# Performance work log

Hardware: AMD Instinct MI355X
Metric: run time of the kernel (lower is better)

## Reference

```python
import jax, jax.numpy as jnp
import numpy as np

FACTOR = 1.0

def _dct_matrix():
    n = 8
    D = np.zeros((n * n, n * n), dtype=np.float32)
    for u in range(n):
        for v in range(n):
            au = 1.0 / np.sqrt(2.0) if u == 0 else 1.0
            av = 1.0 / np.sqrt(2.0) if v == 0 else 1.0
            alpha = au * av * 0.25
            for x in range(n):
                for y in range(n):
                    D[u * n + v, x * n + y] = alpha * np.cos((2 * x + 1) * u * np.pi / 16) * np.cos((2 * y + 1) * v * np.pi / 16)
    return D

def _y_quant_table():
    t = np.array([[16, 11, 10, 16, 24, 40, 51, 61], [12, 12, 14, 19, 26, 58, 60, 55],
                  [14, 13, 16, 24, 40, 57, 69, 56], [14, 17, 22, 29, 51, 87, 80, 62],
                  [18, 22, 37, 56, 68, 109, 103, 77], [24, 35, 55, 64, 81, 104, 113, 92],
                  [49, 64, 78, 87, 103, 121, 120, 101], [72, 92, 95, 98, 112, 100, 103, 99]],
                 dtype=np.float32).T
    return t

def _c_quant_table():
    t = np.full((8, 8), 99, dtype=np.float32)
    t[:4, :4] = np.array([[17, 18, 24, 47], [18, 21, 26, 66], [24, 26, 56, 99], [47, 66, 99, 99]],
                          dtype=np.float32).T
    return t

_D = jnp.asarray(_dct_matrix())          # [64,64]
_QT = jnp.stack([jnp.asarray(_y_quant_table()),
                 jnp.asarray(_c_quant_table()),
                 jnp.asarray(_c_quant_table())], axis=0) * FACTOR  # [3,8,8]

def setup_inputs() -> dict:
    key = jax.random.key(0)
    image = jax.random.uniform(key, (32, 3, 512, 512), dtype=jnp.float32)
    return {"image": image}

def _diffjpeg(image):
    x = jnp.clip(image, 0.0, 1.0)
    B, C, H, W = x.shape  # H, W multiples of 8 -> no padding branch
    r, g, b = x[:, 0], x[:, 1], x[:, 2]
    y = 0.299 * r + 0.587 * g + 0.114 * b
    cb = (b - y) * 0.564 + 0.5
    cr = (r - y) * 0.713 + 0.5
    ycbcr = jnp.stack([y, cb, cr], axis=1)  # [B,3,H,W]
    # blockify into 8x8 tiles
    nh, nw = H // 8, W // 8
    blocks = ycbcr.reshape(B, C, nh, 8, nw, 8).transpose(0, 1, 2, 4, 3, 5)  # [B,C,nh,nw,8,8]
    flat = blocks.reshape(-1, 64) * 255.0 - 128.0
    dct = flat @ _D.T                      # matmul(D, flat.T).T
    dctb = dct.reshape(B, C, nh, nw, 8, 8)
    qte = _QT[None, :, None, None, :, :]   # [1,3,1,1,8,8]
    q = dctb / qte
    q = q + jax.lax.stop_gradient(jnp.round(q) - q)  # STE rounding
    deq = q * qte
    idct = deq.reshape(-1, 64) @ _D        # matmul(D.T, x.T).T
    idct = (idct + 128.0) / 255.0
    img = idct.reshape(B, C, nh, nw, 8, 8).transpose(0, 1, 2, 4, 3, 5).reshape(B, C, H, W)
    yy, ycb, ycr = img[:, 0], img[:, 1] - 0.5, img[:, 2] - 0.5
    rr = yy + 1.403 * ycr
    gg = yy - 0.714 * ycr - 0.344 * ycb
    bb = yy + 1.773 * ycb
    rgb = jnp.clip(jnp.stack([rr, gg, bb], axis=1), 0.0, 1.0)
    return jnp.clip(rgb, 0.0, 1.0)

def reference(image):
    return _diffjpeg(image)
```

## Files before the change

### kernel.cpp

```cpp
#include <hip/hip_runtime.h>

typedef float f32x2 __attribute__((ext_vector_type(2)));

#define K4 0.353553391f
#define K1 0.490392640f
#define K3 0.415734806f
#define K5 0.277785117f
#define K7 0.097545161f
#define K2 0.461939766f
#define K6 0.191341716f

__device__ __align__(16) const float YQT[64] = {
    16.f, 12.f, 14.f, 14.f,  18.f,  24.f,  49.f,  72.f,
    11.f, 12.f, 13.f, 17.f,  22.f,  35.f,  64.f,  92.f,
    10.f, 14.f, 16.f, 22.f,  37.f,  55.f,  78.f,  95.f,
    16.f, 19.f, 24.f, 29.f,  56.f,  64.f,  87.f,  98.f,
    24.f, 26.f, 40.f, 51.f,  68.f,  81.f, 103.f, 112.f,
    40.f, 58.f, 57.f, 87.f, 109.f, 104.f, 121.f, 100.f,
    51.f, 60.f, 69.f, 80.f, 103.f, 113.f, 120.f, 103.f,
    61.f, 55.f, 56.f, 62.f,  77.f,  92.f, 101.f,  99.f
};
__device__ __align__(16) const float RYQT[64] = {
    1.f/16.f, 1.f/12.f, 1.f/14.f, 1.f/14.f, 1.f/18.f,  1.f/24.f,  1.f/49.f,  1.f/72.f,
    1.f/11.f, 1.f/12.f, 1.f/13.f, 1.f/17.f, 1.f/22.f,  1.f/35.f,  1.f/64.f,  1.f/92.f,
    1.f/10.f, 1.f/14.f, 1.f/16.f, 1.f/22.f, 1.f/37.f,  1.f/55.f,  1.f/78.f,  1.f/95.f,
    1.f/16.f, 1.f/19.f, 1.f/24.f, 1.f/29.f, 1.f/56.f,  1.f/64.f,  1.f/87.f,  1.f/98.f,
    1.f/24.f, 1.f/26.f, 1.f/40.f, 1.f/51.f, 1.f/68.f,  1.f/81.f,  1.f/103.f, 1.f/112.f,
    1.f/40.f, 1.f/58.f, 1.f/57.f, 1.f/87.f, 1.f/109.f, 1.f/104.f, 1.f/121.f, 1.f/100.f,
    1.f/51.f, 1.f/60.f, 1.f/69.f, 1.f/80.f, 1.f/103.f, 1.f/113.f, 1.f/120.f, 1.f/103.f,
    1.f/61.f, 1.f/55.f, 1.f/56.f, 1.f/62.f, 1.f/77.f,  1.f/92.f,  1.f/101.f, 1.f/99.f
};
__device__ __align__(16) const float CQ[64] = {
    17.f, 18.f, 24.f, 47.f, 99.f, 99.f, 99.f, 99.f,
    18.f, 21.f, 26.f, 66.f, 99.f, 99.f, 99.f, 99.f,
    24.f, 26.f, 56.f, 99.f, 99.f, 99.f, 99.f, 99.f,
    47.f, 66.f, 99.f, 99.f, 99.f, 99.f, 99.f, 99.f,
    99.f, 99.f, 99.f, 99.f, 99.f, 99.f, 99.f, 99.f,
    99.f, 99.f, 99.f, 99.f, 99.f, 99.f, 99.f, 99.f,
    99.f, 99.f, 99.f, 99.f, 99.f, 99.f, 99.f, 99.f,
    99.f, 99.f, 99.f, 99.f, 99.f, 99.f, 99.f, 99.f
};
__device__ __align__(16) const float RCQ[64] = {
    1.f/17.f, 1.f/18.f, 1.f/24.f, 1.f/47.f, 1.f/99.f, 1.f/99.f, 1.f/99.f, 1.f/99.f,
    1.f/18.f, 1.f/21.f, 1.f/26.f, 1.f/66.f, 1.f/99.f, 1.f/99.f, 1.f/99.f, 1.f/99.f,
    1.f/24.f, 1.f/26.f, 1.f/56.f, 1.f/99.f, 1.f/99.f, 1.f/99.f, 1.f/99.f, 1.f/99.f,
    1.f/47.f, 1.f/66.f, 1.f/99.f, 1.f/99.f, 1.f/99.f, 1.f/99.f, 1.f/99.f, 1.f/99.f,
    1.f/99.f, 1.f/99.f, 1.f/99.f, 1.f/99.f, 1.f/99.f, 1.f/99.f, 1.f/99.f, 1.f/99.f,
    1.f/99.f, 1.f/99.f, 1.f/99.f, 1.f/99.f, 1.f/99.f, 1.f/99.f, 1.f/99.f, 1.f/99.f,
    1.f/99.f, 1.f/99.f, 1.f/99.f, 1.f/99.f, 1.f/99.f, 1.f/99.f, 1.f/99.f, 1.f/99.f,
    1.f/99.f, 1.f/99.f, 1.f/99.f, 1.f/99.f, 1.f/99.f, 1.f/99.f, 1.f/99.f, 1.f/99.f
};

__device__ __forceinline__ float gfma(float a, float b, float c) { return fmaf(a, b, c); }
__device__ __forceinline__ f32x2 gfma(f32x2 a, f32x2 b, f32x2 c) { return __builtin_elementwise_fma(a, b, c); }
__device__ __forceinline__ f32x2 gfma(float a, f32x2 b, f32x2 c) { return __builtin_elementwise_fma((f32x2){a, a}, b, c); }

__device__ __forceinline__ float clamp01(float x) { return __builtin_amdgcn_fmed3f(x, 0.f, 1.f); }

template <typename T>
__device__ __forceinline__ void dct8(const T x[8], T X[8]) {
    const T a0 = x[0] + x[7], a1 = x[1] + x[6], a2 = x[2] + x[5], a3 = x[3] + x[4];
    const T d0 = x[0] - x[7], d1 = x[1] - x[6], d2 = x[2] - x[5], d3 = x[3] - x[4];
    const T e0 = a0 + a3, e1 = a1 + a2, f0 = a0 - a3, f1 = a1 - a2;
    X[0] = K4 * (e0 + e1);
    X[4] = K4 * (e0 - e1);
    X[2] = gfma(K6, f1, K2 * f0);
    X[6] = gfma(-K2, f1, K6 * f0);
    X[1] = gfma(K7, d3, gfma(K5, d2, gfma(K3, d1, K1 * d0)));
    X[3] = gfma(-K5, d3, gfma(-K1, d2, gfma(-K7, d1, K3 * d0)));
    X[5] = gfma(K3, d3, gfma(K7, d2, gfma(-K1, d1, K5 * d0)));
    X[7] = gfma(-K1, d3, gfma(K3, d2, gfma(-K5, d1, K7 * d0)));
}

template <typename T>
__device__ __forceinline__ void idct8(const T X[8], T x[8]) {
    const T g0 = K4 * (X[0] + X[4]);
    const T g1 = K4 * (X[0] - X[4]);
    const T E0 = gfma(K6, X[6], gfma(K2, X[2], g0));
    const T E1 = gfma(-K2, X[6], gfma(K6, X[2], g1));
    const T E2 = gfma(K2, X[6], gfma(-K6, X[2], g1));
    const T E3 = gfma(-K6, X[6], gfma(-K2, X[2], g0));
    const T O0 = gfma(K7, X[7], gfma(K5, X[5], gfma(K3, X[3], K1 * X[1])));
    const T O1 = gfma(-K5, X[7], gfma(-K1, X[5], gfma(-K7, X[3], K3 * X[1])));
    const T O2 = gfma(K3, X[7], gfma(K7, X[5], gfma(-K1, X[3], K5 * X[1])));
    const T O3 = gfma(-K1, X[7], gfma(K3, X[5], gfma(-K5, X[3], K7 * X[1])));
    x[0] = E0 + O0;  x[7] = E0 - O0;
    x[1] = E1 + O1;  x[6] = E1 - O1;
    x[2] = E2 + O2;  x[5] = E2 - O2;
    x[3] = E3 + O3;  x[4] = E3 - O3;
}

__device__ __forceinline__ f32x2 quant2(f32x2 sv, f32x2 qt, f32x2 rq) {
    const f32x2 q0 = sv * rq;
    const f32x2 e  = gfma(-qt, q0, sv);
    const f32x2 q  = gfma(rq, e, q0);
    const f32x2 n  = {rintf(q.x), rintf(q.y)};
    return n * qt;
}

#define SB() __builtin_amdgcn_sched_barrier(0)

#define YW 68
#define CW 70

__global__ __launch_bounds__(128, 8) void diffjpeg_kernel(const float* __restrict__ in,
                                                          float* __restrict__ out)
{
    __shared__ __align__(16) f32x2 lds[2][8][CW];

    const int t  = threadIdx.x;
    const int l  = t & 63;
    const int wv = t >> 6;
    const int b8 = (l >> 3) * 8;
    const int rr = l & 7;

    f32x2 (*plc)[CW] = lds[wv];
    float* ply = (float*)&lds[wv][0][0];

    const int bid  = blockIdx.x;
    const int img  = bid >> 8;
    const int rem  = bid & 255;
    const int trow = rem >> 3;
    const int tcol = rem & 7;
    const size_t HW = (size_t)512 * 512;
    const size_t sbase = (size_t)img * 3 * HW + (size_t)(trow * 16 + wv * 8) * 512 + (size_t)(tcol * 64);
    const float* __restrict__ pin  = in  + sbase + l;
    float* __restrict__       pout = out + sbase + l;

    float rv[8], gv[8], bv[8];
    #pragma unroll
    for (int x = 0; x < 8; ++x) rv[x] = pin[(size_t)x * 512];
    #pragma unroll
    for (int x = 0; x < 8; ++x) gv[x] = pin[HW + (size_t)x * 512];
    #pragma unroll
    for (int x = 0; x < 8; ++x) bv[x] = pin[2 * HW + (size_t)x * 512];

    float yv[8];
    f32x2 cc[8];
    #pragma unroll
    for (int x = 0; x < 8; ++x) {
        const float r = clamp01(rv[x]);
        const float g = clamp01(gv[x]);
        const float b = clamp01(bv[x]);
        const float Y = fmaf(76.245f, r, fmaf(149.685f, g, 29.07f * b));
        yv[x] = Y - 128.f;
        const f32x2 tbr = gfma(255.f, (f32x2){b, r}, (f32x2){-Y, -Y});
        cc[x] = gfma((f32x2){0.564f, 0.713f}, tbr, (f32x2){-0.5f, -0.5f});
    }

    float sy[8];
    {
        float X0[8];
        dct8(yv, X0);
        #pragma unroll
        for (int u = 0; u < 8; ++u) ply[u * YW + l] = X0[u];
        SB();

        {
            const float4* yq4  = (const float4*)&YQT[rr * 8];
            const float4* ryq4 = (const float4*)&RYQT[rr * 8];
            const float4 yqa = yq4[0],  yqb = yq4[1];
            const float4 rya = ryq4[0], ryb = ryq4[1];
            const float yq[8]  = {yqa.x, yqa.y, yqa.z, yqa.w, yqb.x, yqb.y, yqb.z, yqb.w};
            const float ryq[8] = {rya.x, rya.y, rya.z, rya.w, ryb.x, ryb.y, ryb.z, ryb.w};

            float4* rp = (float4*)(ply + rr * YW + b8);
            const float4 a0 = rp[0];
            const float4 a1 = rp[1];
            const float T[8] = {a0.x, a0.y, a0.z, a0.w, a1.x, a1.y, a1.z, a1.w};
            float S[8];
            dct8(T, S);
            float Dq[8];
            #pragma unroll
            for (int i = 0; i < 4; ++i) {
                const f32x2 d = quant2((f32x2){S[2*i], S[2*i+1]},
                                       (f32x2){yq[2*i], yq[2*i+1]},
                                       (f32x2){ryq[2*i], ryq[2*i+1]});
                Dq[2*i] = d.x; Dq[2*i+1] = d.y;
            }
            float o[8];
            idct8(Dq, o);
            rp[0] = make_float4(o[0], o[1], o[2], o[3]);
            rp[1] = make_float4(o[4], o[5], o[6], o[7]);
        }
        SB();

        float Xy[8];
        #pragma unroll
        for (int u = 0; u < 8; ++u) Xy[u] = ply[u * YW + l];
        idct8(Xy, sy);
    }
    SB();

    f32x2 sc[8];
    {
        f32x2 XC[8];
        dct8(cc, XC);
        #pragma unroll
        for (int u = 0; u < 8; ++u) plc[u][l] = XC[u];
        SB();

        {
            const float4* cq4  = (const float4*)&CQ[rr * 8];
            const float4* rcq4 = (const float4*)&RCQ[rr * 8];
            const float4 cqa = cq4[0],  cqb = cq4[1];
            const float4 rca = rcq4[0], rcb4 = rcq4[1];
            const float cq[8]  = {cqa.x, cqa.y, cqa.z, cqa.w, cqb.x, cqb.y, cqb.z, cqb.w};
            const float rcq[8] = {rca.x, rca.y, rca.z, rca.w, rcb4.x, rcb4.y, rcb4.z, rcb4.w};

            float4* rp = (float4*)&plc[rr][b8];
            const float4 p0 = rp[0], p1 = rp[1], p2 = rp[2], p3 = rp[3];
            const f32x2 T[8] = {{p0.x, p0.y}, {p0.z, p0.w}, {p1.x, p1.y}, {p1.z, p1.w},
                                {p2.x, p2.y}, {p2.z, p2.w}, {p3.x, p3.y}, {p3.z, p3.w}};
            f32x2 S[8];
            dct8(T, S);
            f32x2 Dq[8];
            #pragma unroll
            for (int v = 0; v < 8; ++v)
                Dq[v] = quant2(S[v], (f32x2){cq[v], cq[v]}, (f32x2){rcq[v], rcq[v]});
            f32x2 o[8];
            idct8(Dq, o);
            rp[0] = make_float4(o[0].x, o[0].y, o[1].x, o[1].y);
            rp[1] = make_float4(o[2].x, o[2].y, o[3].x, o[3].y);
            rp[2] = make_float4(o[4].x, o[4].y, o[5].x, o[5].y);
            rp[3] = make_float4(o[6].x, o[6].y, o[7].x, o[7].y);
        }
        SB();

        f32x2 Xc[8];
        #pragma unroll
        for (int u = 0; u < 8; ++u) Xc[u] = plc[u][l];
        idct8(Xc, sc);
    }

    {
        constexpr float inv255 = 1.0f / 255.0f;
        constexpr float Kr = 0.504711754f;
        constexpr float Kg = 0.499886280f;
        constexpr float Kb = 0.505437240f;
        #pragma unroll
        for (int x = 0; x < 8; ++x) {
            const float scb = sc[x].x;
            const float scr = sc[x].y;
            const f32x2 inner = gfma((f32x2){1.403f, 1.773f}, (f32x2){scr, scb},
                                     (f32x2){sy[x], sy[x]});
            const f32x2 rb = gfma(inv255, inner, (f32x2){Kr, Kb});
            const float gg = fmaf(inv255, fmaf(-0.714f, scr, fmaf(-0.344f, scb, sy[x])), Kg);
            __builtin_nontemporal_store(clamp01(rb.x), pout + (size_t)x * 512);
            __builtin_nontemporal_store(clamp01(gg),   pout + HW + (size_t)x * 512);
            __builtin_nontemporal_store(clamp01(rb.y), pout + 2 * HW + (size_t)x * 512);
        }
    }
}

extern "C" void kernel_launch(void* const* d_in, const int* in_sizes, int n_in,
                              void* d_out, int out_size, void* d_ws, size_t ws_size,
                              hipStream_t stream) {
    const float* in = (const float*)d_in[0];
    float* out = (float*)d_out;
    const int B = in_sizes[0] / (3 * 512 * 512);
    const int grid = B * 256;
    diffjpeg_kernel<<<grid, 128, 0, stream>>>(in, out);
}
```

Before: 37.49 us.

## Process two pixel columns per thread with 8-byte vector loads and larger blocks

Each thread now handles two adjacent columns, so global loads and stores become 64-bit float2 accesses. Work per wave doubles to 128 columns and the block grows to 256 threads covering a 32x128 tile. The luma and chroma LDS transposes are reorganised to pack two blocks per lane. The aim is fewer memory instructions and more work per thread, at the cost of more registers, a larger LDS footprint and possible LDS bank conflicts from the new strided access pattern.

```diff
diff --git a/kernel.cpp b/kernel.cpp
--- a/kernel.cpp
+++ b/kernel.cpp
@@ -56,6 +56,7 @@
 __device__ __forceinline__ f32x2 gfma(float a, f32x2 b, f32x2 c) { return __builtin_elementwise_fma((f32x2){a, a}, b, c); }
 
 __device__ __forceinline__ float clamp01(float x) { return __builtin_amdgcn_fmed3f(x, 0.f, 1.f); }
+__device__ __forceinline__ f32x2 clamp2(f32x2 v) { return (f32x2){clamp01(v.x), clamp01(v.y)}; }
 
 template <typename T>
 __device__ __forceinline__ void dct8(const T x[8], T X[8]) {
@@ -100,60 +101,59 @@
 
 #define SB() __builtin_amdgcn_sched_barrier(0)
 
-#define YW 68
-#define CW 70
-
-__global__ __launch_bounds__(128, 8) void diffjpeg_kernel(const float* __restrict__ in,
+#define YW2 132
+#define CW2 132
+
+__global__ __launch_bounds__(256, 4) void diffjpeg_kernel(const float* __restrict__ in,
                                                           float* __restrict__ out)
 {
-    __shared__ __align__(16) f32x2 lds[2][8][CW];
+    __shared__ __align__(16) f32x2 lds[4][8][CW2];
 
     const int t  = threadIdx.x;
     const int l  = t & 63;
     const int wv = t >> 6;
-    const int b8 = (l >> 3) * 8;
     const int rr = l & 7;
-
-    f32x2 (*plc)[CW] = lds[wv];
+    const int bc = l >> 3;
+
+    f32x2 (*plc)[CW2] = lds[wv];
     float* ply = (float*)&lds[wv][0][0];
 
     const int bid  = blockIdx.x;
-    const int img  = bid >> 8;
-    const int rem  = bid & 255;
-    const int trow = rem >> 3;
-    const int tcol = rem & 7;
+    const int img  = bid >> 6;
+    const int rem  = bid & 63;
+    const int trow = rem >> 2;
+    const int tcol = rem & 3;
     const size_t HW = (size_t)512 * 512;
-    const size_t sbase = (size_t)img * 3 * HW + (size_t)(trow * 16 + wv * 8) * 512 + (size_t)(tcol * 64);
-    const float* __restrict__ pin  = in  + sbase + l;
-    float* __restrict__       pout = out + sbase + l;
-
-    float rv[8], gv[8], bv[8];
-    #pragma unroll
-    for (int x = 0; x < 8; ++x) rv[x] = pin[(size_t)x * 512];
-    #pragma unroll
-    for (int x = 0; x < 8; ++x) gv[x] = pin[HW + (size_t)x * 512];
-    #pragma unroll
-    for (int x = 0; x < 8; ++x) bv[x] = pin[2 * HW + (size_t)x * 512];
-
-    float yv[8];
-    f32x2 cc[8];
+    const size_t sbase = (size_t)img * 3 * HW + (size_t)(trow * 32 + wv * 8) * 512 + (size_t)(tcol * 128);
+    const float* __restrict__ pin  = in  + sbase + 2 * l;
+    float* __restrict__       pout = out + sbase + 2 * l;
+
+    f32x2 rv[8], gv[8], bv[8];
+    #pragma unroll
+    for (int x = 0; x < 8; ++x) rv[x] = *(const f32x2*)(pin + (size_t)x * 512);
+    #pragma unroll
+    for (int x = 0; x < 8; ++x) gv[x] = *(const f32x2*)(pin + HW + (size_t)x * 512);
+    #pragma unroll
+    for (int x = 0; x < 8; ++x) bv[x] = *(const f32x2*)(pin + 2 * HW + (size_t)x * 512);
+
+    f32x2 yv[8], cbv[8], crv[8];
     #pragma unroll
     for (int x = 0; x < 8; ++x) {
-        const float r = clamp01(rv[x]);
-        const float g = clamp01(gv[x]);
-        const float b = clamp01(bv[x]);
-        const float Y = fmaf(76.245f, r, fmaf(149.685f, g, 29.07f * b));
+        const f32x2 r = clamp2(rv[x]);
+        const f32x2 g = clamp2(gv[x]);
+        const f32x2 b = clamp2(bv[x]);
+        const f32x2 Y = gfma(76.245f, r, gfma(149.685f, g, 29.07f * b));
         yv[x] = Y - 128.f;
-        const f32x2 tbr = gfma(255.f, (f32x2){b, r}, (f32x2){-Y, -Y});
-        cc[x] = gfma((f32x2){0.564f, 0.713f}, tbr, (f32x2){-0.5f, -0.5f});
-    }
-
-    float sy[8];
+        cbv[x] = gfma(0.564f, gfma(255.f, b, -Y), (f32x2){-0.5f, -0.5f});
+        crv[x] = gfma(0.713f, gfma(255.f, r, -Y), (f32x2){-0.5f, -0.5f});
+    }
+
+    f32x2 sy[8];
     {
-        float X0[8];
+        f32x2 X0[8];
         dct8(yv, X0);
         #pragma unroll
-        for (int u = 0; u < 8; ++u) ply[u * YW + l] = X0[u];
+        for (int u = 0; u < 8; ++u) *(f32x2*)&ply[u * YW2 + 2 * l] = X0[u];
         SB();
 
         {
@@ -164,40 +164,38 @@
             const float yq[8]  = {yqa.x, yqa.y, yqa.z, yqa.w, yqb.x, yqb.y, yqb.z, yqb.w};
             const float ryq[8] = {rya.x, rya.y, rya.z, rya.w, ryb.x, ryb.y, ryb.z, ryb.w};
 
-            float4* rp = (float4*)(ply + rr * YW + b8);
-            const float4 a0 = rp[0];
-            const float4 a1 = rp[1];
-            const float T[8] = {a0.x, a0.y, a0.z, a0.w, a1.x, a1.y, a1.z, a1.w};
-            float S[8];
+            float* base1 = ply + rr * YW2 + bc * 8;
+            f32x2 T[8];
+            #pragma unroll
+            for (int y = 0; y < 8; ++y) T[y] = (f32x2){base1[y], base1[y + 64]};
+            f32x2 S[8];
             dct8(T, S);
-            float Dq[8];
-            #pragma unroll
-            for (int i = 0; i < 4; ++i) {
-                const f32x2 d = quant2((f32x2){S[2*i], S[2*i+1]},
-                                       (f32x2){yq[2*i], yq[2*i+1]},
-                                       (f32x2){ryq[2*i], ryq[2*i+1]});
-                Dq[2*i] = d.x; Dq[2*i+1] = d.y;
-            }
-            float o[8];
+            f32x2 Dq[8];
+            #pragma unroll
+            for (int v = 0; v < 8; ++v)
+                Dq[v] = quant2(S[v], (f32x2){yq[v], yq[v]}, (f32x2){ryq[v], ryq[v]});
+            f32x2 o[8];
             idct8(Dq, o);
-            rp[0] = make_float4(o[0], o[1], o[2], o[3]);
-            rp[1] = make_float4(o[4], o[5], o[6], o[7]);
-        }
-        SB();
-
-        float Xy[8];
-        #pragma unroll
-        for (int u = 0; u < 8; ++u) Xy[u] = ply[u * YW + l];
+            #pragma unroll
+            for (int y = 0; y < 8; ++y) { base1[y] = o[y].x; base1[y + 64] = o[y].y; }
+        }
+        SB();
+
+        f32x2 Xy[8];
+        #pragma unroll
+        for (int u = 0; u < 8; ++u) Xy[u] = *(f32x2*)&ply[u * YW2 + 2 * l];
         idct8(Xy, sy);
     }
     SB();
 
-    f32x2 sc[8];
+    f32x2 sc0[8], sc1[8];
     {
-        f32x2 XC[8];
-        dct8(cc, XC);
-        #pragma unroll
-        for (int u = 0; u < 8; ++u) plc[u][l] = XC[u];
+        f32x2 XB[8], XR[8];
+        dct8(cbv, XB);
+        dct8(crv, XR);
+        #pragma unroll
+        for (int u = 0; u < 8; ++u)
+            *(float4*)&plc[u][2 * l] = make_float4(XB[u].x, XR[u].x, XB[u].y, XR[u].y);
         SB();
 
         {
@@ -208,29 +206,38 @@
             const float cq[8]  = {cqa.x, cqa.y, cqa.z, cqa.w, cqb.x, cqb.y, cqb.z, cqb.w};
             const float rcq[8] = {rca.x, rca.y, rca.z, rca.w, rcb4.x, rcb4.y, rcb4.z, rcb4.w};
 
-            float4* rp = (float4*)&plc[rr][b8];
-            const float4 p0 = rp[0], p1 = rp[1], p2 = rp[2], p3 = rp[3];
-            const f32x2 T[8] = {{p0.x, p0.y}, {p0.z, p0.w}, {p1.x, p1.y}, {p1.z, p1.w},
-                                {p2.x, p2.y}, {p2.z, p2.w}, {p3.x, p3.y}, {p3.z, p3.w}};
-            f32x2 S[8];
-            dct8(T, S);
-            f32x2 Dq[8];
-            #pragma unroll
-            for (int v = 0; v < 8; ++v)
-                Dq[v] = quant2(S[v], (f32x2){cq[v], cq[v]}, (f32x2){rcq[v], rcq[v]});
-            f32x2 o[8];
-            idct8(Dq, o);
-            rp[0] = make_float4(o[0].x, o[0].y, o[1].x, o[1].y);
-            rp[1] = make_float4(o[2].x, o[2].y, o[3].x, o[3].y);
-            rp[2] = make_float4(o[4].x, o[4].y, o[5].x, o[5].y);
-            rp[3] = make_float4(o[6].x, o[6].y, o[7].x, o[7].y);
-        }
-        SB();
-
-        f32x2 Xc[8];
-        #pragma unroll
-        for (int u = 0; u < 8; ++u) Xc[u] = plc[u][l];
-        idct8(Xc, sc);
+            f32x2* cbase = &plc[rr][bc * 8];
+            #pragma unroll
+            for (int j = 0; j < 2; ++j) {
+                float4* rp = (float4*)(cbase + j * 64);
+                const float4 p0 = rp[0], p1 = rp[1], p2 = rp[2], p3 = rp[3];
+                const f32x2 T[8] = {{p0.x, p0.y}, {p0.z, p0.w}, {p1.x, p1.y}, {p1.z, p1.w},
+                                    {p2.x, p2.y}, {p2.z, p2.w}, {p3.x, p3.y}, {p3.z, p3.w}};
+                f32x2 S[8];
+                dct8(T, S);
+                f32x2 Dq[8];
+                #pragma unroll
+                for (int v = 0; v < 8; ++v)
+                    Dq[v] = quant2(S[v], (f32x2){cq[v], cq[v]}, (f32x2){rcq[v], rcq[v]});
+                f32x2 o[8];
+                idct8(Dq, o);
+                rp[0] = make_float4(o[0].x, o[0].y, o[1].x, o[1].y);
+                rp[1] = make_float4(o[2].x, o[2].y, o[3].x, o[3].y);
+                rp[2] = make_float4(o[4].x, o[4].y, o[5].x, o[5].y);
+                rp[3] = make_float4(o[6].x, o[6].y, o[7].x, o[7].y);
+            }
+        }
+        SB();
+
+        f32x2 Xc0[8], Xc1[8];
+        #pragma unroll
+        for (int u = 0; u < 8; ++u) {
+            const float4 q = *(const float4*)&plc[u][2 * l];
+            Xc0[u] = (f32x2){q.x, q.y};
+            Xc1[u] = (f32x2){q.z, q.w};
+        }
+        idct8(Xc0, sc0);
+        idct8(Xc1, sc1);
     }
 
     {
@@ -240,15 +247,21 @@
         constexpr float Kb = 0.505437240f;
         #pragma unroll
         for (int x = 0; x < 8; ++x) {
-            const float scb = sc[x].x;
-            const float scr = sc[x].y;
-            const f32x2 inner = gfma((f32x2){1.403f, 1.773f}, (f32x2){scr, scb},
-                                     (f32x2){sy[x], sy[x]});
-            const f32x2 rb = gfma(inv255, inner, (f32x2){Kr, Kb});
-            const float gg = fmaf(inv255, fmaf(-0.714f, scr, fmaf(-0.344f, scb, sy[x])), Kg);
-            __builtin_nontemporal_store(clamp01(rb.x), pout + (size_t)x * 512);
-            __builtin_nontemporal_store(clamp01(gg),   pout + HW + (size_t)x * 512);
-            __builtin_nontemporal_store(clamp01(rb.y), pout + 2 * HW + (size_t)x * 512);
+            const float y0 = sy[x].x, y1 = sy[x].y;
+            const float cb0 = sc0[x].x, cr0 = sc0[x].y;
+            const float cb1 = sc1[x].x, cr1 = sc1[x].y;
+            const f32x2 in0 = gfma((f32x2){1.403f, 1.773f}, (f32x2){cr0, cb0}, (f32x2){y0, y0});
+            const f32x2 rb0 = gfma(inv255, in0, (f32x2){Kr, Kb});
+            const float g0  = fmaf(inv255, fmaf(-0.714f, cr0, fmaf(-0.344f, cb0, y0)), Kg);
+            const f32x2 in1 = gfma((f32x2){1.403f, 1.773f}, (f32x2){cr1, cb1}, (f32x2){y1, y1});
+            const f32x2 rb1 = gfma(inv255, in1, (f32x2){Kr, Kb});
+            const float g1  = fmaf(inv255, fmaf(-0.714f, cr1, fmaf(-0.344f, cb1, y1)), Kg);
+            const f32x2 Rst = (f32x2){clamp01(rb0.x), clamp01(rb1.x)};
+            const f32x2 Gst = (f32x2){clamp01(g0),   clamp01(g1)};
+            const f32x2 Bst = (f32x2){clamp01(rb0.y), clamp01(rb1.y)};
+            __builtin_nontemporal_store(Rst, (f32x2*)(pout + (size_t)x * 512));
+            __builtin_nontemporal_store(Gst, (f32x2*)(pout + HW + (size_t)x * 512));
+            __builtin_nontemporal_store(Bst, (f32x2*)(pout + 2 * HW + (size_t)x * 512));
         }
     }
 }
@@ -259,6 +272,6 @@
     const float* in = (const float*)d_in[0];
     float* out = (float*)d_out;
     const int B = in_sizes[0] / (3 * 512 * 512);
-    const int grid = B * 256;
-    diffjpeg_kernel<<<grid, 128, 0, stream>>>(in, out);
-}
+    const int grid = B * 64;
+    diffjpeg_kernel<<<grid, 256, 0, stream>>>(in, out);
+}
```

Result: faster. 34.92 us (-6.9%).
